# Performance work log

Measured on AMD Instinct MI355X. Metric: run time of the kernel, lower is better.

## Reference

```python
import jax, jax.numpy as jnp
import numpy as np

B, L, D, H = 4, 2048, 512, 8
HD = D // H
NEG = -1e9


def setup_inputs() -> dict:
    key = jax.random.key(0)
    ks = jax.random.split(key, 11)
    s = 1.0 / np.sqrt(D)
    inp = {
        "q": jax.random.normal(ks[0], (B, L, D), jnp.float32),
        "k": jax.random.normal(ks[1], (B, L, D), jnp.float32),
        "v": jax.random.normal(ks[2], (B, L, D), jnp.float32),
        "mask": jnp.broadcast_to(jnp.tril(jnp.ones((L, L), jnp.int32)), (B, L, L)),
        "Wq": jax.random.normal(ks[3], (D, D), jnp.float32) * s,
        "bq": jax.random.normal(ks[4], (D,), jnp.float32) * s,
        "Wk": jax.random.normal(ks[5], (D, D), jnp.float32) * s,
        "bk": jax.random.normal(ks[6], (D,), jnp.float32) * s,
        "Wv": jax.random.normal(ks[7], (D, D), jnp.float32) * s,
        "bv": jax.random.normal(ks[8], (D,), jnp.float32) * s,
        "Wo": jax.random.normal(ks[9], (D, D), jnp.float32) * s,
        "bo": jax.random.normal(ks[10], (D,), jnp.float32) * s,
    }
    return inp


def reference(q, k, v, mask, Wq, bq, Wk, bk, Wv, bv, Wo, bo):
    # Linear projections (torch Linear: x @ W.T + b)
    Q = (q @ Wq.T + bq).reshape(B, L, H, HD).transpose(0, 2, 1, 3)  # [B,H,L,hd]
    K = (k @ Wk.T + bk).reshape(B, L, H, HD).transpose(0, 2, 1, 3)
    V = (v @ Wv.T + bv).reshape(B, L, H, HD).transpose(0, 2, 1, 3)
    # scaled dot-product attention with masked_fill(mask==0, -1e9)
    score = jnp.einsum('bhqd,bhkd->bhqk', Q, K) / jnp.sqrt(jnp.float32(HD))
    score = jnp.where(mask[:, None, :, :] == 0, NEG, score)
    attn = jax.nn.softmax(score, axis=-1)
    ctx = jnp.einsum('bhqk,bhkd->bhqd', attn, V)  # [B,H,L,hd]
    ctx = ctx.transpose(0, 2, 1, 3).reshape(B, L, D)
    return ctx @ Wo.T + bo
```

## Files before the change

### kernel.cpp

```cpp
#include <hip/hip_runtime.h>
#include <hip/hip_bf16.h>
#include <math.h>

constexpr int Bc  = 4;
constexpr int Lc  = 2048;
constexpr int Dc  = 512;
constexpr int Hc  = 8;
constexpr int HDc = 64;

constexpr int GK = Dc;
constexpr int BK = 64;

typedef __attribute__((ext_vector_type(8))) short bf16x8;
typedef __attribute__((ext_vector_type(4))) float f32x4;

static __device__ __forceinline__ short f2bf(float x) {
    __hip_bfloat16 h = __float2bfloat16(x);
    return (short)__builtin_bit_cast(unsigned short, h);
}

static __device__ __forceinline__ void gload_lds16(const void* g, void* l) {
    __builtin_amdgcn_global_load_lds(
        (const __attribute__((address_space(1))) void*)g,
        (__attribute__((address_space(3))) void*)l, 16, 0, 0);
}

__global__ __launch_bounds__(256)
void cast_all(const float* __restrict__ q, const float* __restrict__ k,
              const float* __restrict__ v, const float* __restrict__ wq,
              const float* __restrict__ wk, const float* __restrict__ wv,
              const float* __restrict__ wo, short* __restrict__ dst) {
    const size_t i = ((size_t)blockIdx.x * 256 + threadIdx.x) * 8;
    const float* src; size_t off;
    if      (i <  4194304) { src = q;  off = i; }
    else if (i <  8388608) { src = k;  off = i -  4194304; }
    else if (i < 12582912) { src = v;  off = i -  8388608; }
    else if (i < 12845056) { src = wq; off = i - 12582912; }
    else if (i < 13107200) { src = wk; off = i - 12845056; }
    else if (i < 13369344) { src = wv; off = i - 13107200; }
    else                   { src = wo; off = i - 13369344; }
    const float4 a = *(const float4*)(src + off);
    const float4 b = *(const float4*)(src + off + 4);
    bf16x8 o;
    o[0] = f2bf(a.x); o[1] = f2bf(a.y); o[2] = f2bf(a.z); o[3] = f2bf(a.w);
    o[4] = f2bf(b.x); o[5] = f2bf(b.y); o[6] = f2bf(b.z); o[7] = f2bf(b.w);
    *(bf16x8*)(dst + i) = o;
}

template<int BM, int BN, int WMT, int WNT>
__device__ __forceinline__ void gemm_tile(const short* __restrict__ A,
                                          const short* __restrict__ W,
                                          short* As, short* Bs,
                                          f32x4 (&acc)[WMT][WNT],
                                          int m0, int n0) {
    const int tid  = threadIdx.x;
    const int w    = tid >> 6;
    const int lane = tid & 63;
    const int low4 = lane & 15;
    const int quad = lane >> 4;
    const int wm   = w & 1, wn = w >> 1;
    const int lrow = lane >> 3;
    const int lchk = (lane & 7) * 8;

    for (int k0 = 0; k0 < GK; k0 += BK) {
#pragma unroll
        for (int i = 0; i < BM / 32; ++i) {
            const int r0 = i * 32 + w * 8;
            gload_lds16(A + (size_t)(m0 + r0 + lrow) * GK + k0 + lchk, As + r0 * BK);
        }
#pragma unroll
        for (int i = 0; i < BN / 32; ++i) {
            const int r0 = i * 32 + w * 8;
            gload_lds16(W + (size_t)(n0 + r0 + lrow) * GK + k0 + lchk, Bs + r0 * BK);
        }
        __syncthreads();
#pragma unroll
        for (int ks = 0; ks < 2; ++ks) {
            bf16x8 af[WMT], bfr[WNT];
#pragma unroll
            for (int mi = 0; mi < WMT; ++mi)
                af[mi] = *(const bf16x8*)(As + (wm * WMT * 16 + mi * 16 + low4) * BK + ks * 32 + quad * 8);
#pragma unroll
            for (int ni = 0; ni < WNT; ++ni)
                bfr[ni] = *(const bf16x8*)(Bs + (wn * WNT * 16 + ni * 16 + low4) * BK + ks * 32 + quad * 8);
#pragma unroll
            for (int mi = 0; mi < WMT; ++mi)
#pragma unroll
                for (int ni = 0; ni < WNT; ++ni)
                    acc[mi][ni] = __builtin_amdgcn_mfma_f32_16x16x32_bf16(af[mi], bfr[ni], acc[mi][ni], 0, 0, 0);
        }
        __syncthreads();
    }
}

__global__ __launch_bounds__(256)
void qkv_gemm(const short* __restrict__ Xq, const short* __restrict__ Xk,
              const short* __restrict__ Xv, const short* __restrict__ Wcat,
              const float* __restrict__ bq, const float* __restrict__ bk,
              const float* __restrict__ bv,
              short* __restrict__ Qw, short* __restrict__ Kw, short* __restrict__ Vw) {
    __shared__ __align__(16) short Smem[128 * 138];
    short* As = Smem;
    short* Bs = Smem + 8192;
    short* Ts = Smem;

    const int tid = threadIdx.x;
    const int n0 = blockIdx.x * 128;
    const int m0 = blockIdx.y * 128;
    const int z  = n0 >> 9;
    const short* A    = (z == 0) ? Xq : (z == 1) ? Xk : Xv;
    const float* bias = (z == 0) ? bq : (z == 1) ? bk : bv;

    f32x4 acc[4][4];
#pragma unroll
    for (int mi = 0; mi < 4; ++mi)
#pragma unroll
        for (int ni = 0; ni < 4; ++ni) acc[mi][ni] = (f32x4){0.f, 0.f, 0.f, 0.f};

    gemm_tile<128, 128, 4, 4>(A, Wcat, As, Bs, acc, m0, n0);

    const int lane = tid & 63, w = tid >> 6;
    const int low4 = lane & 15, quad = lane >> 4;
    const int wm = w & 1, wn = w >> 1;

    if (z < 2) {
        short* Y = (z == 0) ? Qw : Kw;
#pragma unroll
        for (int mi = 0; mi < 4; ++mi)
#pragma unroll
            for (int ni = 0; ni < 4; ++ni)
#pragma unroll
                for (int r = 0; r < 4; ++r) {
                    const int rowL = wm * 64 + mi * 16 + quad * 4 + r;
                    const int colL = wn * 64 + ni * 16 + low4;
                    const int c    = (n0 & 511) + colL;
                    Ts[rowL * 138 + colL] = f2bf(acc[mi][ni][r] + bias[c]);
                }
        __syncthreads();
        const int j = tid & 7;
        const int b = m0 >> 11;
#pragma unroll
        for (int it = 0; it < 8; ++it) {
            const int slot = it * 32 + (tid >> 3);
            const int row  = slot >> 1, half = slot & 1;
            const int c0 = (n0 & 511) + half * 64;
            const int h  = c0 >> 6;
            const int l  = (m0 & 2047) + row;
            short* dst = Y + (((size_t)b * Hc + h) * Lc + l) * HDc + j * 8;
            *(bf16x8*)dst = *(const bf16x8*)(Ts + row * 138 + half * 64 + j * 8);
        }
    } else {
#pragma unroll
        for (int mi = 0; mi < 4; ++mi)
#pragma unroll
            for (int ni = 0; ni < 4; ++ni)
#pragma unroll
                for (int r = 0; r < 4; ++r) {
                    const int rowL = wm * 64 + mi * 16 + quad * 4 + r;
                    const int colL = wn * 64 + ni * 16 + low4;
                    const int c    = (n0 + colL) & 511;
                    Ts[colL * 136 + rowL] = f2bf(acc[mi][ni][r] + bias[c]);
                }
        __syncthreads();
        const int hdl = tid >> 1, seg = tid & 1;
        const int c  = (n0 + hdl) & 511;
        const int h  = c >> 6, hd = c & 63;
        const int b  = m0 >> 11, l0 = (m0 & 2047) + seg * 64;
        short* dst = Vw + (((size_t)b * Hc + h) * HDc + hd) * Lc + l0;
        const short* srcT = Ts + hdl * 136 + seg * 64;
#pragma unroll
        for (int j = 0; j < 8; ++j)
            *(bf16x8*)(dst + j * 8) = *(const bf16x8*)(srcT + j * 8);
    }
}

__global__ __launch_bounds__(256)
void out_gemm(const short* __restrict__ A, const short* __restrict__ W,
              const float* __restrict__ bias, float* __restrict__ Y) {
    __shared__ __align__(16) float SmemF[64 * 132];
    short* As = (short*)SmemF;
    short* Bs = As + 64 * BK;
    float* Tf = SmemF;

    const int tid = threadIdx.x;
    const int n0 = blockIdx.x * 128;
    const int m0 = blockIdx.y * 64;

    f32x4 acc[2][4];
#pragma unroll
    for (int mi = 0; mi < 2; ++mi)
#pragma unroll
        for (int ni = 0; ni < 4; ++ni) acc[mi][ni] = (f32x4){0.f, 0.f, 0.f, 0.f};

    gemm_tile<64, 128, 2, 4>(A, W, As, Bs, acc, m0, n0);

    const int lane = tid & 63, w = tid >> 6;
    const int low4 = lane & 15, quad = lane >> 4;
    const int wm = w & 1, wn = w >> 1;
#pragma unroll
    for (int mi = 0; mi < 2; ++mi)
#pragma unroll
        for (int ni = 0; ni < 4; ++ni)
#pragma unroll
            for (int r = 0; r < 4; ++r) {
                const int rowL = wm * 32 + mi * 16 + quad * 4 + r;
                const int colL = wn * 64 + ni * 16 + low4;
                Tf[rowL * 132 + colL] = acc[mi][ni][r] + bias[n0 + colL];
            }
    __syncthreads();

    const int c = (tid & 31) * 4;
#pragma unroll
    for (int p = 0; p < 8; ++p) {
        const int row = p * 8 + (tid >> 5);
        *(float4*)(Y + (size_t)(m0 + row) * Dc + n0 + c) =
            *(const float4*)(Tf + row * 132 + c);
    }
}

__global__ __launch_bounds__(256)
void flash_attn(const short* __restrict__ Qb, const short* __restrict__ Kb,
                const short* __restrict__ VTb, short* __restrict__ ctx) {
    __shared__ __align__(16) short Kf[2][4096];
    __shared__ __align__(16) short Vf[2][4096];
    __shared__ __align__(16) short Ps[4][16 * 72];

    const int tid  = threadIdx.x;
    const int w    = tid >> 6;
    const int lane = tid & 63;
    const int low4 = lane & 15;
    const int quad = lane >> 4;

    const int bh = blockIdx.x & 31;
    const int qt = 31 - (blockIdx.x >> 5);
    const int q0w = qt * 64 + w * 16;

    const short* Qg = Qb  + (size_t)bh * Lc * HDc;
    const short* Kg = Kb  + (size_t)bh * Lc * HDc;
    const short* Vg = VTb + (size_t)bh * HDc * Lc;

    const bf16x8 qa0 = *(const bf16x8*)(Qg + (size_t)(q0w + low4) * HDc + quad * 8);
    const bf16x8 qa1 = *(const bf16x8*)(Qg + (size_t)(q0w + low4) * HDc + 32 + quad * 8);

    f32x4 o[4];
    float lp[4] = {0.f, 0.f, 0.f, 0.f};
#pragma unroll
    for (int i = 0; i < 4; ++i) o[i] = (f32x4){0.f, 0.f, 0.f, 0.f};

#define STAGE(KT_, BUF_)                                                        \
    {                                                                           \
        _Pragma("unroll")                                                       \
        for (int p = 0; p < 2; ++p) {                                           \
            const int dc = w + 4 * p;                                           \
            gload_lds16(Kg + (size_t)((KT_) + lane) * HDc + dc * 8,             \
                        &Kf[BUF_][(dc * 64 + lane) * 8]);                       \
            gload_lds16(Vg + (size_t)lane * Lc + (KT_) + dc * 8,                \
                        &Vf[BUF_][(dc * 64 + lane) * 8]);                       \
        }                                                                       \
    }

    STAGE(0, 0);
    __syncthreads();

    for (int t = 0; t <= qt; ++t) {
        const int buf = t & 1;
        if (t < qt) STAGE((t + 1) * 64, buf ^ 1);

        f32x4 s[4];
#pragma unroll
        for (int nt = 0; nt < 4; ++nt) s[nt] = (f32x4){0.f, 0.f, 0.f, 0.f};
#pragma unroll
        for (int ks = 0; ks < 2; ++ks) {
            const bf16x8 qa = ks ? qa1 : qa0;
#pragma unroll
            for (int nt = 0; nt < 4; ++nt) {
                const bf16x8 kf = *(const bf16x8*)(&Kf[buf][((ks * 4 + quad) * 64 + nt * 16 + low4) * 8]);
                s[nt] = __builtin_amdgcn_mfma_f32_16x16x32_bf16(qa, kf, s[nt], 0, 0, 0);
            }
        }

        short* pw = Ps[w];
        const int kt = t * 64;
        if (t < qt) {
#pragma unroll
            for (int nt = 0; nt < 4; ++nt)
#pragma unroll
                for (int r = 0; r < 4; ++r) {
                    const float p = __expf(s[nt][r] * 0.125f);
                    lp[r] += p;
                    pw[(quad * 4 + r) * 72 + nt * 16 + low4] = f2bf(p);
                }
        } else {
#pragma unroll
            for (int nt = 0; nt < 4; ++nt)
#pragma unroll
                for (int r = 0; r < 4; ++r) {
                    const int qrow = q0w + quad * 4 + r;
                    const int col  = kt + nt * 16 + low4;
                    float p = __expf(s[nt][r] * 0.125f);
                    if (col > qrow) p = 0.f;
                    lp[r] += p;
                    pw[(quad * 4 + r) * 72 + nt * 16 + low4] = f2bf(p);
                }
        }

        __asm__ volatile("s_waitcnt lgkmcnt(0)" ::: "memory");

#pragma unroll
        for (int ks = 0; ks < 2; ++ks) {
            const bf16x8 pf = *(const bf16x8*)(pw + low4 * 72 + ks * 32 + quad * 8);
#pragma unroll
            for (int nt = 0; nt < 4; ++nt) {
                const bf16x8 vf = *(const bf16x8*)(&Vf[buf][((ks * 4 + quad) * 64 + nt * 16 + low4) * 8]);
                o[nt] = __builtin_amdgcn_mfma_f32_16x16x32_bf16(pf, vf, o[nt], 0, 0, 0);
            }
        }

        __syncthreads();
    }

#pragma unroll
    for (int off = 1; off < 16; off <<= 1)
#pragma unroll
        for (int r = 0; r < 4; ++r)
            lp[r] += __shfl_xor(lp[r], off, 64);

    const int b = bh >> 3, h = bh & 7;
#pragma unroll
    for (int r = 0; r < 4; ++r) {
        const float inv = 1.f / lp[r];
        const int q = q0w + quad * 4 + r;
#pragma unroll
        for (int nt = 0; nt < 4; ++nt)
            ctx[(size_t)(b * Lc + q) * Dc + h * HDc + nt * 16 + low4] = f2bf(o[nt][r] * inv);
    }
#undef STAGE
}

extern "C" void kernel_launch(void* const* d_in, const int* in_sizes, int n_in,
                              void* d_out, int out_size, void* d_ws, size_t ws_size,
                              hipStream_t stream) {
    const float* q  = (const float*)d_in[0];
    const float* k  = (const float*)d_in[1];
    const float* v  = (const float*)d_in[2];
    const float* Wq = (const float*)d_in[4];
    const float* bq = (const float*)d_in[5];
    const float* Wk = (const float*)d_in[6];
    const float* bk = (const float*)d_in[7];
    const float* Wv = (const float*)d_in[8];
    const float* bv = (const float*)d_in[9];
    const float* Wo = (const float*)d_in[10];
    const float* bo = (const float*)d_in[11];
    float* out = (float*)d_out;

    const size_t per = (size_t)Bc * Lc * Dc;
    const size_t wsz = (size_t)Dc * Dc;
    short* Xq  = (short*)d_ws;
    short* Xk  = Xq + per;
    short* Xv  = Xk + per;
    short* Wcat = Xv + per;
    short* Wob = Wcat + 3 * wsz;
    short* Qw  = Wob + wsz;
    short* Kw  = Qw + per;
    short* Vw  = Kw + per;
    short* Cw  = Vw + per;

    cast_all<<<6656, 256, 0, stream>>>(q, k, v, Wq, Wk, Wv, Wo, Xq);

    qkv_gemm<<<dim3(12, 64), 256, 0, stream>>>(Xq, Xk, Xv, Wcat,
                                               bq, bk, bv, Qw, Kw, Vw);

    flash_attn<<<1024, 256, 0, stream>>>(Qw, Kw, Vw, Cw);

    out_gemm<<<dim3(4, 128), 256, 0, stream>>>(Cw, Wob, bo, out);
}
```

Measured before the change: 238.5 us.

## Fuse fp32-to-bf16 activation cast into QKV GEMM tile loads

Drops the separate cast pass over the q/k/v activations. The QKV GEMM now loads fp32 activation tiles straight into LDS in a k-quad-major layout and converts them to bf16 when reading MMA fragments. Only the weights are still pre-cast, using a packed bf16x2 conversion helper. This removes a full read/write round trip of the activations and a kernel launch, in exchange for twice the LDS footprint and load traffic for the A tile and conversion work in the inner loop, which is repeated across the 12 column blocks.

```diff
diff --git a/kernel.cpp b/kernel.cpp
--- a/kernel.cpp
+++ b/kernel.cpp
@@ -19,6 +19,15 @@
     return (short)__builtin_bit_cast(unsigned short, h);
 }
 
+static __device__ __forceinline__ bf16x8 pack8(float4 a, float4 b) {
+    union { __hip_bfloat162 h2[4]; bf16x8 v; } u;
+    u.h2[0] = __float22bfloat162_rn({a.x, a.y});
+    u.h2[1] = __float22bfloat162_rn({a.z, a.w});
+    u.h2[2] = __float22bfloat162_rn({b.x, b.y});
+    u.h2[3] = __float22bfloat162_rn({b.z, b.w});
+    return u.v;
+}
+
 static __device__ __forceinline__ void gload_lds16(const void* g, void* l) {
     __builtin_amdgcn_global_load_lds(
         (const __attribute__((address_space(1))) void*)g,
@@ -26,89 +35,42 @@
 }
 
 __global__ __launch_bounds__(256)
-void cast_all(const float* __restrict__ q, const float* __restrict__ k,
-              const float* __restrict__ v, const float* __restrict__ wq,
-              const float* __restrict__ wk, const float* __restrict__ wv,
-              const float* __restrict__ wo, short* __restrict__ dst) {
+void cast_w(const float* __restrict__ wq, const float* __restrict__ wk,
+            const float* __restrict__ wv, const float* __restrict__ wo,
+            short* __restrict__ dst) {
     const size_t i = ((size_t)blockIdx.x * 256 + threadIdx.x) * 8;
     const float* src; size_t off;
-    if      (i <  4194304) { src = q;  off = i; }
-    else if (i <  8388608) { src = k;  off = i -  4194304; }
-    else if (i < 12582912) { src = v;  off = i -  8388608; }
-    else if (i < 12845056) { src = wq; off = i - 12582912; }
-    else if (i < 13107200) { src = wk; off = i - 12845056; }
-    else if (i < 13369344) { src = wv; off = i - 13107200; }
-    else                   { src = wo; off = i - 13369344; }
+    if      (i < 262144) { src = wq; off = i; }
+    else if (i < 524288) { src = wk; off = i - 262144; }
+    else if (i < 786432) { src = wv; off = i - 524288; }
+    else                 { src = wo; off = i - 786432; }
     const float4 a = *(const float4*)(src + off);
     const float4 b = *(const float4*)(src + off + 4);
-    bf16x8 o;
-    o[0] = f2bf(a.x); o[1] = f2bf(a.y); o[2] = f2bf(a.z); o[3] = f2bf(a.w);
-    o[4] = f2bf(b.x); o[5] = f2bf(b.y); o[6] = f2bf(b.z); o[7] = f2bf(b.w);
-    *(bf16x8*)(dst + i) = o;
-}
-
-template<int BM, int BN, int WMT, int WNT>
-__device__ __forceinline__ void gemm_tile(const short* __restrict__ A,
-                                          const short* __restrict__ W,
-                                          short* As, short* Bs,
-                                          f32x4 (&acc)[WMT][WNT],
-                                          int m0, int n0) {
-    const int tid  = threadIdx.x;
+    *(bf16x8*)(dst + i) = pack8(a, b);
+}
+
+__global__ __launch_bounds__(256)
+void qkv_gemm(const float* __restrict__ Xq, const float* __restrict__ Xk,
+              const float* __restrict__ Xv, const short* __restrict__ Wcat,
+              const float* __restrict__ bq, const float* __restrict__ bk,
+              const float* __restrict__ bv,
+              short* __restrict__ Qw, short* __restrict__ Kw, short* __restrict__ Vw) {
+    __shared__ __align__(16) short Smem[24576];
+    float* Asf = (float*)Smem;
+    short* Bs  = Smem + 16384;
+    short* Ts  = Smem;
+
+    const int tid = threadIdx.x;
     const int w    = tid >> 6;
     const int lane = tid & 63;
     const int low4 = lane & 15;
     const int quad = lane >> 4;
     const int wm   = w & 1, wn = w >> 1;
-    const int lrow = lane >> 3;
-    const int lchk = (lane & 7) * 8;
-
-    for (int k0 = 0; k0 < GK; k0 += BK) {
-#pragma unroll
-        for (int i = 0; i < BM / 32; ++i) {
-            const int r0 = i * 32 + w * 8;
-            gload_lds16(A + (size_t)(m0 + r0 + lrow) * GK + k0 + lchk, As + r0 * BK);
-        }
-#pragma unroll
-        for (int i = 0; i < BN / 32; ++i) {
-            const int r0 = i * 32 + w * 8;
-            gload_lds16(W + (size_t)(n0 + r0 + lrow) * GK + k0 + lchk, Bs + r0 * BK);
-        }
-        __syncthreads();
-#pragma unroll
-        for (int ks = 0; ks < 2; ++ks) {
-            bf16x8 af[WMT], bfr[WNT];
-#pragma unroll
-            for (int mi = 0; mi < WMT; ++mi)
-                af[mi] = *(const bf16x8*)(As + (wm * WMT * 16 + mi * 16 + low4) * BK + ks * 32 + quad * 8);
-#pragma unroll
-            for (int ni = 0; ni < WNT; ++ni)
-                bfr[ni] = *(const bf16x8*)(Bs + (wn * WNT * 16 + ni * 16 + low4) * BK + ks * 32 + quad * 8);
-#pragma unroll
-            for (int mi = 0; mi < WMT; ++mi)
-#pragma unroll
-                for (int ni = 0; ni < WNT; ++ni)
-                    acc[mi][ni] = __builtin_amdgcn_mfma_f32_16x16x32_bf16(af[mi], bfr[ni], acc[mi][ni], 0, 0, 0);
-        }
-        __syncthreads();
-    }
-}
-
-__global__ __launch_bounds__(256)
-void qkv_gemm(const short* __restrict__ Xq, const short* __restrict__ Xk,
-              const short* __restrict__ Xv, const short* __restrict__ Wcat,
-              const float* __restrict__ bq, const float* __restrict__ bk,
-              const float* __restrict__ bv,
-              short* __restrict__ Qw, short* __restrict__ Kw, short* __restrict__ Vw) {
-    __shared__ __align__(16) short Smem[128 * 138];
-    short* As = Smem;
-    short* Bs = Smem + 8192;
-    short* Ts = Smem;
-
-    const int tid = threadIdx.x;
+
     const int n0 = blockIdx.x * 128;
     const int m0 = blockIdx.y * 128;
     const int z  = n0 >> 9;
-    const short* A    = (z == 0) ? Xq : (z == 1) ? Xk : Xv;
+    const float* Ain  = (z == 0) ? Xq : (z == 1) ? Xk : Xv;
     const float* bias = (z == 0) ? bq : (z == 1) ? bk : bv;
 
     f32x4 acc[4][4];
@@ -117,11 +79,46 @@
 #pragma unroll
         for (int ni = 0; ni < 4; ++ni) acc[mi][ni] = (f32x4){0.f, 0.f, 0.f, 0.f};
 
-    gemm_tile<128, 128, 4, 4>(A, Wcat, As, Bs, acc, m0, n0);
-
-    const int lane = tid & 63, w = tid >> 6;
-    const int low4 = lane & 15, quad = lane >> 4;
-    const int wm = w & 1, wn = w >> 1;
+    const int lrowB = lane >> 3;
+    const int lchkB = (lane & 7) * 8;
+
+    for (int k0 = 0; k0 < GK; k0 += BK) {
+#pragma unroll
+        for (int j = 0; j < 8; ++j) {
+            const int S   = w * 8 + j;
+            const int kq  = S >> 1;
+            const int r64 = (S & 1) * 64;
+            gload_lds16(Ain + (size_t)(m0 + r64 + lane) * GK + k0 + kq * 4,
+                        Asf + (size_t)S * 256);
+        }
+#pragma unroll
+        for (int i = 0; i < 4; ++i) {
+            const int r0 = i * 32 + w * 8;
+            gload_lds16(Wcat + (size_t)(n0 + r0 + lrowB) * GK + k0 + lchkB,
+                        Bs + r0 * BK);
+        }
+        __syncthreads();
+
+#pragma unroll
+        for (int ks = 0; ks < 2; ++ks) {
+            bf16x8 af[4], bfr[4];
+#pragma unroll
+            for (int mi = 0; mi < 4; ++mi) {
+                const float4* ap = (const float4*)Asf
+                    + (ks * 8 + quad * 2) * 128 + wm * 64 + mi * 16 + low4;
+                af[mi] = pack8(ap[0], ap[128]);
+            }
+#pragma unroll
+            for (int ni = 0; ni < 4; ++ni)
+                bfr[ni] = *(const bf16x8*)(Bs + (wn * 64 + ni * 16 + low4) * BK + ks * 32 + quad * 8);
+#pragma unroll
+            for (int mi = 0; mi < 4; ++mi)
+#pragma unroll
+                for (int ni = 0; ni < 4; ++ni)
+                    acc[mi][ni] = __builtin_amdgcn_mfma_f32_16x16x32_bf16(af[mi], bfr[ni], acc[mi][ni], 0, 0, 0);
+        }
+        __syncthreads();
+    }
 
     if (z < 2) {
         short* Y = (z == 0) ? Qw : Kw;
@@ -183,6 +180,14 @@
     float* Tf = SmemF;
 
     const int tid = threadIdx.x;
+    const int w    = tid >> 6;
+    const int lane = tid & 63;
+    const int low4 = lane & 15;
+    const int quad = lane >> 4;
+    const int wm   = w & 1, wn = w >> 1;
+    const int lrow = lane >> 3;
+    const int lchk = (lane & 7) * 8;
+
     const int n0 = blockIdx.x * 128;
     const int m0 = blockIdx.y * 64;
 
@@ -192,11 +197,36 @@
 #pragma unroll
         for (int ni = 0; ni < 4; ++ni) acc[mi][ni] = (f32x4){0.f, 0.f, 0.f, 0.f};
 
-    gemm_tile<64, 128, 2, 4>(A, W, As, Bs, acc, m0, n0);
-
-    const int lane = tid & 63, w = tid >> 6;
-    const int low4 = lane & 15, quad = lane >> 4;
-    const int wm = w & 1, wn = w >> 1;
+    for (int k0 = 0; k0 < GK; k0 += BK) {
+#pragma unroll
+        for (int i = 0; i < 2; ++i) {
+            const int r0 = i * 32 + w * 8;
+            gload_lds16(A + (size_t)(m0 + r0 + lrow) * GK + k0 + lchk, As + r0 * BK);
+        }
+#pragma unroll
+        for (int i = 0; i < 4; ++i) {
+            const int r0 = i * 32 + w * 8;
+            gload_lds16(W + (size_t)(n0 + r0 + lrow) * GK + k0 + lchk, Bs + r0 * BK);
+        }
+        __syncthreads();
+#pragma unroll
+        for (int ks = 0; ks < 2; ++ks) {
+            bf16x8 af[2], bfr[4];
+#pragma unroll
+            for (int mi = 0; mi < 2; ++mi)
+                af[mi] = *(const bf16x8*)(As + (wm * 32 + mi * 16 + low4) * BK + ks * 32 + quad * 8);
+#pragma unroll
+            for (int ni = 0; ni < 4; ++ni)
+                bfr[ni] = *(const bf16x8*)(Bs + (wn * 64 + ni * 16 + low4) * BK + ks * 32 + quad * 8);
+#pragma unroll
+            for (int mi = 0; mi < 2; ++mi)
+#pragma unroll
+                for (int ni = 0; ni < 4; ++ni)
+                    acc[mi][ni] = __builtin_amdgcn_mfma_f32_16x16x32_bf16(af[mi], bfr[ni], acc[mi][ni], 0, 0, 0);
+        }
+        __syncthreads();
+    }
+
 #pragma unroll
     for (int mi = 0; mi < 2; ++mi)
 #pragma unroll
@@ -355,19 +385,16 @@
 
     const size_t per = (size_t)Bc * Lc * Dc;
     const size_t wsz = (size_t)Dc * Dc;
-    short* Xq  = (short*)d_ws;
-    short* Xk  = Xq + per;
-    short* Xv  = Xk + per;
-    short* Wcat = Xv + per;
-    short* Wob = Wcat + 3 * wsz;
-    short* Qw  = Wob + wsz;
-    short* Kw  = Qw + per;
-    short* Vw  = Kw + per;
-    short* Cw  = Vw + per;
-
-    cast_all<<<6656, 256, 0, stream>>>(q, k, v, Wq, Wk, Wv, Wo, Xq);
-
-    qkv_gemm<<<dim3(12, 64), 256, 0, stream>>>(Xq, Xk, Xv, Wcat,
+    short* Wcat = (short*)d_ws;
+    short* Wob  = Wcat + 3 * wsz;
+    short* Qw   = Wob + wsz;
+    short* Kw   = Qw + per;
+    short* Vw   = Kw + per;
+    short* Cw   = Vw + per;
+
+    cast_w<<<512, 256, 0, stream>>>(Wq, Wk, Wv, Wo, Wcat);
+
+    qkv_gemm<<<dim3(12, 64), 256, 0, stream>>>(q, k, v, Wcat,
                                                bq, bk, bv, Qw, Kw, Vw);
 
     flash_attn<<<1024, 256, 0, stream>>>(Qw, Kw, Vw, Cw);
```

After: 251.2 us. +5.3%, slower.
